# Performance work log

Measured on AMD Instinct MI355X. Metric: run time of the kernel, lower is better.

The kernel has to match this reference:

```python
import jax, jax.numpy as jnp
import numpy as np

HID = 512       # hidden_dim (embed/LSTM input)
HDE = 512       # hidden_dim_de == attn_channels (required by conv_att channel count)
NCLS = 7000
LSEQ = 40
B = 128
FH, FW = 8, 32


def setup_inputs() -> dict:
    key = jax.random.key(0)
    ks = jax.random.split(key, 16)
    s = 0.05
    inp = {
        "hidden_en": jax.random.normal(ks[0], (1, B, HID), jnp.float32),
        "x_em": jax.random.normal(ks[1], (B, HDE, FH, FW), jnp.float32),
        "att_x_em": jax.random.normal(ks[2], (B, FH * FW, HDE), jnp.float32),
        "target": jax.random.randint(ks[3], (B, LSEQ), 0, NCLS),
        "feature_h": FH,
        "feature_w": FW,
        # parameters
        "embed_w": jax.random.normal(ks[4], (NCLS, HID), jnp.float32) * s,
        "W_ih": jax.random.normal(ks[5], (4 * HDE, HID), jnp.float32) * s,   # LSTMCell input weights (i,f,g,o)
        "W_hh": jax.random.normal(ks[6], (4 * HDE, HDE), jnp.float32) * s,
        "b_ih": jax.random.normal(ks[7], (4 * HDE,), jnp.float32) * s,
        "b_hh": jax.random.normal(ks[8], (4 * HDE,), jnp.float32) * s,
        "hem_w": jax.random.normal(ks[9], (HDE, HDE), jnp.float32) * s,     # 1x1 conv h_em as matrix
        "hem_b": jax.random.normal(ks[10], (HDE,), jnp.float32) * s,
        "attw_w": jax.random.normal(ks[11], (HDE,), jnp.float32) * s,       # 1x1 conv conv_att -> 1 channel
        "attw_b": jax.random.normal(ks[12], (), jnp.float32) * s,
        "lin_w": jax.random.normal(ks[13], (NCLS, HDE + HDE), jnp.float32) * s,
        "lin_b": jax.random.normal(ks[14], (NCLS,), jnp.float32) * s,
    }
    return inp


def _decode(hidden_en, x_em, att_x_em, target, embed_w, W_ih, W_hh, b_ih, b_hh,
            hem_w, hem_b, attw_w, attw_b, lin_w, lin_b):
    L = target.shape[1]
    # teacher-forced inputs: step 0 uses hidden_en[-1], step t>=1 uses embed(target[:, t-1])
    xt0 = hidden_en[-1]                                   # [B, HID]
    xts = jnp.concatenate([xt0[None], jnp.transpose(embed_w[target[:, : L - 1]], (1, 0, 2))], axis=0)  # [L,B,HID]
    xg_all = jnp.einsum('lbi,gi->lbg', xts, W_ih) + b_ih  # precompute input gates [L,B,4H]
    Bn = x_em.shape[0]
    h0 = jnp.zeros((Bn, HDE), x_em.dtype)
    c0 = jnp.zeros((Bn, HDE), x_em.dtype)

    def step(carry, xg):
        h, c = carry
        gates = xg + h @ W_hh.T + b_hh
        i, f, g, o = jnp.split(gates, 4, axis=-1)
        c = jax.nn.sigmoid(f) * c + jax.nn.sigmoid(i) * jnp.tanh(g)
        h = jax.nn.sigmoid(o) * jnp.tanh(c)
        # additive attention (dropout treated as identity for determinism)
        hem = h @ hem_w.T + hem_b                          # [B, C]
        feat = jnp.tanh(x_em + hem[:, :, None, None])      # [B, C, H, W]
        feat_att = jnp.einsum('bchw,c->bhw', feat, attw_w) + attw_b
        alpha = jax.nn.softmax(feat_att.reshape(Bn, -1), axis=-1)  # [B, HW]
        att = jnp.einsum('bn,bnd->bd', alpha, att_x_em)    # [B, C]
        scores = jax.nn.log_softmax(jnp.concatenate([h, att], -1) @ lin_w.T + lin_b)
        return (h, c), scores

    _, ys = jax.lax.scan(step, (h0, c0), xg_all)           # ys: [L, B, NCLS]
    return jnp.transpose(ys, (1, 0, 2))                    # [B, L, NCLS]


def reference(hidden_en, x_em, att_x_em, target, feature_h, feature_w,
              embed_w, W_ih, W_hh, b_ih, b_hh, hem_w, hem_b, attw_w, attw_b,
              lin_w, lin_b):
    return _decode(hidden_en, x_em, att_x_em, target, embed_w, W_ih, W_hh,
                   b_ih, b_hh, hem_w, hem_b, attw_w, attw_b, lin_w, lin_b)
```

## Files before the change

kernel.cpp:

```cpp
#include <hip/hip_runtime.h>

#define B_    128
#define HIDD  512
#define NCLS  7000
#define NPAD  7040
#define LSEQ  40
#define MROWS 5120
#define TT    10

typedef __attribute__((ext_vector_type(8))) short bf16x8;
typedef __attribute__((ext_vector_type(4))) float f32x4;

__device__ __forceinline__ unsigned short f2bf(float x) {
  union { float f; unsigned u; } v; v.f = x;
  unsigned r = v.u + 0x7fffu + ((v.u >> 16) & 1u);
  return (unsigned short)(r >> 16);
}
__device__ __forceinline__ float bf2f(unsigned short h) {
  union { unsigned u; float f; } v; v.u = ((unsigned)h) << 16;
  return v.f;
}
__device__ __forceinline__ float sigm(float x) { return 1.f / (1.f + __expf(-x)); }
__device__ __forceinline__ float tanh_f(float x) {
  float e = __expf(2.f * x);
  return 1.f - 2.f / (e + 1.f);
}
__device__ __forceinline__ float rcp_f(float x) { return __builtin_amdgcn_rcpf(x); }

__global__ __launch_bounds__(256) void k_cvt(const float* __restrict__ src,
                                             unsigned short* __restrict__ dst, int n4) {
  int i = blockIdx.x * 256 + threadIdx.x;
  if (i >= n4) return;
  float4 v = ((const float4*)src)[i];
  ushort4 o; o.x = f2bf(v.x); o.y = f2bf(v.y); o.z = f2bf(v.z); o.w = f2bf(v.w);
  ((ushort4*)dst)[i] = o;
}

__global__ __launch_bounds__(256) void k_expcvt(const float* __restrict__ src,
                                                unsigned short* __restrict__ dst, int n4) {
  int i = blockIdx.x * 256 + threadIdx.x;
  if (i >= n4) return;
  float4 v = ((const float4*)src)[i];
  ushort4 o;
  o.x = f2bf(__expf(2.f * v.x)); o.y = f2bf(__expf(2.f * v.y));
  o.z = f2bf(__expf(2.f * v.z)); o.w = f2bf(__expf(2.f * v.w));
  ((ushort4*)dst)[i] = o;
}

__global__ __launch_bounds__(256) void k_linpad(const float* __restrict__ lw,
                                                unsigned short* __restrict__ dst) {
  int i = blockIdx.x * 256 + threadIdx.x;
  int e = i * 4;
  int row = e >> 10;
  ushort4 o;
  if (row < NCLS) {
    float4 v = *(const float4*)(lw + (size_t)row * 1024 + (e & 1023));
    o.x = f2bf(v.x); o.y = f2bf(v.y); o.z = f2bf(v.z); o.w = f2bf(v.w);
  } else { o.x = 0; o.y = 0; o.z = 0; o.w = 0; }
  ((ushort4*)dst)[i] = o;
}

__global__ __launch_bounds__(256) void k_xts(const float* __restrict__ hidden_en,
                                             const float* __restrict__ embed_w,
                                             const int* __restrict__ target,
                                             unsigned short* __restrict__ xts) {
  int i = blockIdx.x * 256 + threadIdx.x;
  int e = i * 4;
  int r = e >> 9, col = e & 511;
  int l = r >> 7, b = r & 127;
  const float* src;
  if (l == 0) src = hidden_en + b * 512 + col;
  else        src = embed_w + (size_t)target[b * LSEQ + (l - 1)] * 512 + col;
  float4 v = *(const float4*)src;
  ushort4 o; o.x = f2bf(v.x); o.y = f2bf(v.y); o.z = f2bf(v.z); o.w = f2bf(v.w);
  ((ushort4*)xts)[i] = o;
}

template <int MODE>
__global__ __launch_bounds__(256) void k_gemm(const unsigned short* __restrict__ A, int lda,
                                              const unsigned short* __restrict__ Bw, int ldb,
                                              const float* __restrict__ bias,
                                              void* __restrict__ outp, int ldc, int K) {
  __shared__ __align__(16) unsigned short As[128 * 32];
  __shared__ __align__(16) unsigned short Bs[128 * 32];
  const int tid = threadIdx.x;
  const int lane = tid & 63, wid = tid >> 6;
  const int wm = wid >> 1, wn = wid & 1;
  const int quad = lane >> 4, l16 = lane & 15;
  const int m0 = blockIdx.x * 128, n0 = blockIdx.y * 128;
  f32x4 acc[4][4];
#pragma unroll
  for (int i = 0; i < 4; i++)
#pragma unroll
    for (int j = 0; j < 4; j++) acc[i][j] = (f32x4){0.f, 0.f, 0.f, 0.f};

  const int r0 = tid >> 2, kq0 = (tid & 3) * 8;
  for (int k0 = 0; k0 < K; k0 += 32) {
#pragma unroll
    for (int s = 0; s < 2; s++) {
      int row = r0 + s * 64;
      *(bf16x8*)(As + row * 32 + kq0) = *(const bf16x8*)(A + (size_t)(m0 + row) * lda + k0 + kq0);
      *(bf16x8*)(Bs + row * 32 + kq0) = *(const bf16x8*)(Bw + (size_t)(n0 + row) * ldb + k0 + kq0);
    }
    __syncthreads();
    bf16x8 af[4], bfr[4];
#pragma unroll
    for (int i = 0; i < 4; i++)
      af[i] = *(const bf16x8*)(As + (wm * 64 + i * 16 + l16) * 32 + quad * 8);
#pragma unroll
    for (int j = 0; j < 4; j++)
      bfr[j] = *(const bf16x8*)(Bs + (wn * 64 + j * 16 + l16) * 32 + quad * 8);
#pragma unroll
    for (int i = 0; i < 4; i++)
#pragma unroll
      for (int j = 0; j < 4; j++)
        acc[i][j] = __builtin_amdgcn_mfma_f32_16x16x32_bf16(af[i], bfr[j], acc[i][j], 0, 0, 0);
    __syncthreads();
  }
#pragma unroll
  for (int i = 0; i < 4; i++) {
    int mbase = m0 + wm * 64 + i * 16 + quad * 4;
#pragma unroll
    for (int j = 0; j < 4; j++) {
      int n = n0 + wn * 64 + j * 16 + l16;
#pragma unroll
      for (int r = 0; r < 4; r++) {
        float v = acc[i][j][r];
        int m = mbase + r;
        if (MODE == 0) {
          ((unsigned short*)outp)[(size_t)m * ldc + n] = f2bf(v + bias[n]);
        } else if (MODE == 3) {
          ((float*)outp)[(size_t)m * ldc + n] = __expf(2.f * (v + bias[n]));
        } else {
          if (n < NCLS) {
            int t = m >> 7, b = m & 127;
            ((float*)outp)[((size_t)(b * LSEQ + t)) * NCLS + n] = v + bias[n];
          }
        }
      }
    }
  }
}

__global__ __launch_bounds__(256) void k_gates(const float* __restrict__ h_prev,
                                               float* __restrict__ h_new,
                                               float* __restrict__ c_buf,
                                               const unsigned short* __restrict__ xg,
                                               const float* __restrict__ W_hh,
                                               const float* __restrict__ b_hh,
                                               unsigned short* __restrict__ hatt, int t) {
  __shared__ float h_s[16][68];
  __shared__ float W_s[64][68];
  const int tid = threadIdx.x;
  const int mt = blockIdx.x >> 5, jt = blockIdx.x & 31;
  const int m0 = mt * 16, j0 = jt * 16;
  const int mi = tid >> 4, ji = tid & 15;
  float a0 = 0.f, a1 = 0.f, a2 = 0.f, a3 = 0.f;
  if (t > 0) {
    for (int k0 = 0; k0 < 512; k0 += 64) {
      {
        int row = tid >> 4, c4 = (tid & 15) * 4;
        *(float4*)&h_s[row][c4] = *(const float4*)&h_prev[(m0 + row) * 512 + k0 + c4];
      }
#pragma unroll
      for (int w = 0; w < 4; w++) {
        int lin = w * 256 + tid;
        int row = lin >> 4, c4 = (lin & 15) * 4;
        int g = row >> 4, jj = row & 15;
        *(float4*)&W_s[row][c4] = *(const float4*)&W_hh[(size_t)((g << 9) + j0 + jj) * 512 + k0 + c4];
      }
      __syncthreads();
#pragma unroll 4
      for (int kk = 0; kk < 64; kk += 4) {
        float4 hv = *(const float4*)&h_s[mi][kk];
        float4 w0 = *(const float4*)&W_s[ji][kk];
        float4 w1 = *(const float4*)&W_s[16 + ji][kk];
        float4 w2 = *(const float4*)&W_s[32 + ji][kk];
        float4 w3 = *(const float4*)&W_s[48 + ji][kk];
        a0 += hv.x * w0.x + hv.y * w0.y + hv.z * w0.z + hv.w * w0.w;
        a1 += hv.x * w1.x + hv.y * w1.y + hv.z * w1.z + hv.w * w1.w;
        a2 += hv.x * w2.x + hv.y * w2.y + hv.z * w2.z + hv.w * w2.w;
        a3 += hv.x * w3.x + hv.y * w3.y + hv.z * w3.z + hv.w * w3.w;
      }
      __syncthreads();
    }
  }
  const int m = m0 + mi, j = j0 + ji;
  const size_t r = (size_t)t * 128 + m;
  a0 += bf2f(xg[r * 2048 + j])          + b_hh[j];
  a1 += bf2f(xg[r * 2048 + 512 + j])    + b_hh[512 + j];
  a2 += bf2f(xg[r * 2048 + 1024 + j])   + b_hh[1024 + j];
  a3 += bf2f(xg[r * 2048 + 1536 + j])   + b_hh[1536 + j];
  float ig = sigm(a0), fg = sigm(a1), gg = tanh_f(a2), og = sigm(a3);
  float c_old = (t > 0) ? c_buf[m * 512 + j] : 0.f;
  float c = fg * c_old + ig * gg;
  float h = og * tanh_f(c);
  c_buf[m * 512 + j] = c;
  h_new[m * 512 + j] = h;
  hatt[r * 1024 + j] = f2bf(h);
}

__global__ __launch_bounds__(256) void k_feat(const float* __restrict__ Eh,
                                              const unsigned short* __restrict__ Ex,
                                              const float* __restrict__ attw_w,
                                              float* __restrict__ s_all) {
  __shared__ float EhL[TT][512];
  __shared__ float wL[512];
  const int tid = threadIdx.x;
  const int tg = blockIdx.x >> 7, b = blockIdx.x & 127;
  const int t0 = tg * TT;
  for (int i = tid * 4; i < TT * 512; i += 1024) {
    int t = i >> 9, c = i & 511;
    *(float4*)&EhL[t][c] = *(const float4*)&Eh[((size_t)(t0 + t) * 128 + b) * 512 + c];
  }
  if (tid < 128) *(float4*)&wL[tid * 4] = *(const float4*)&attw_w[tid * 4];
  __syncthreads();
  const int p = tid;
  const unsigned short* xp = Ex + (size_t)b * 512 * 256 + p;
  float acc[TT];
#pragma unroll
  for (int t = 0; t < TT; t++) acc[t] = 0.f;
  for (int c0 = 0; c0 < 512; c0 += 4) {
    float ex0 = bf2f(xp[(size_t)(c0 + 0) * 256]);
    float ex1 = bf2f(xp[(size_t)(c0 + 1) * 256]);
    float ex2 = bf2f(xp[(size_t)(c0 + 2) * 256]);
    float ex3 = bf2f(xp[(size_t)(c0 + 3) * 256]);
    float4 wv = *(const float4*)&wL[c0];
#pragma unroll
    for (int t = 0; t < TT; t++) {
      float4 eh = *(const float4*)&EhL[t][c0];
      acc[t] = __builtin_fmaf(wv.x, rcp_f(__builtin_fmaf(ex0, eh.x, 1.f)), acc[t]);
      acc[t] = __builtin_fmaf(wv.y, rcp_f(__builtin_fmaf(ex1, eh.y, 1.f)), acc[t]);
      acc[t] = __builtin_fmaf(wv.z, rcp_f(__builtin_fmaf(ex2, eh.z, 1.f)), acc[t]);
      acc[t] = __builtin_fmaf(wv.w, rcp_f(__builtin_fmaf(ex3, eh.w, 1.f)), acc[t]);
    }
  }
#pragma unroll
  for (int t = 0; t < TT; t++)
    s_all[((size_t)(t0 + t) * 128 + b) * 256 + p] = -2.f * acc[t];
}

__global__ __launch_bounds__(256) void k_att(const float* __restrict__ s_all,
                                             const float* __restrict__ atx,
                                             unsigned short* __restrict__ hatt) {
  __shared__ float sL[40][257];
  __shared__ float zinv[40];
  const int tid = threadIdx.x;
  const int b = blockIdx.x >> 1, dh = blockIdx.x & 1;
  for (int i = tid; i < 40 * 256; i += 256) {
    int t = i >> 8, p = i & 255;
    sL[t][p] = s_all[((size_t)t * 128 + b) * 256 + p];
  }
  __syncthreads();
  if (tid < 40) {
    int t = tid;
    float mx = -1e30f;
    for (int p = 0; p < 256; p++) mx = fmaxf(mx, sL[t][p]);
    float z = 0.f;
    for (int p = 0; p < 256; p++) { float e = __expf(sL[t][p] - mx); sL[t][p] = e; z += e; }
    zinv[t] = 1.f / z;
  }
  __syncthreads();
  float acc[40];
#pragma unroll
  for (int t = 0; t < 40; t++) acc[t] = 0.f;
  const int d = dh * 256 + tid;
  const float* ap = atx + (size_t)b * 256 * 512 + d;
  for (int p = 0; p < 256; p++) {
    float av = ap[(size_t)p * 512];
#pragma unroll
    for (int t = 0; t < 40; t++) acc[t] += sL[t][p] * av;
  }
#pragma unroll
  for (int t = 0; t < 40; t++) {
    float v = acc[t] * zinv[t];
    hatt[((size_t)t * 128 + b) * 1024 + 512 + d] = f2bf(v);
  }
}

__global__ __launch_bounds__(256) void k_lsm(float* __restrict__ out) {
  __shared__ float buf[7000];
  __shared__ float red[256];
  const int tid = threadIdx.x;
  float* pr = out + (size_t)blockIdx.x * NCLS;
  for (int i = tid * 4; i < NCLS; i += 1024)
    *(float4*)&buf[i] = *(const float4*)&pr[i];
  __syncthreads();
  float mx = -1e30f;
  for (int i = tid; i < NCLS; i += 256) mx = fmaxf(mx, buf[i]);
  red[tid] = mx; __syncthreads();
  for (int s = 128; s > 0; s >>= 1) { if (tid < s) red[tid] = fmaxf(red[tid], red[tid + s]); __syncthreads(); }
  mx = red[0]; __syncthreads();
  float sum = 0.f;
  for (int i = tid; i < NCLS; i += 256) sum += __expf(buf[i] - mx);
  red[tid] = sum; __syncthreads();
  for (int s = 128; s > 0; s >>= 1) { if (tid < s) red[tid] += red[tid + s]; __syncthreads(); }
  float lse = mx + __logf(red[0]);
  for (int i = tid * 4; i < NCLS; i += 1024) {
    float4 v = *(const float4*)&buf[i];
    v.x -= lse; v.y -= lse; v.z -= lse; v.w -= lse;
    *(float4*)&pr[i] = v;
  }
}

extern "C" void kernel_launch(void* const* d_in, const int* in_sizes, int n_in,
                              void* d_out, int out_size, void* d_ws, size_t ws_size,
                              hipStream_t stream) {
  const float* hidden_en = (const float*)d_in[0];
  const float* x_em      = (const float*)d_in[1];
  const float* att_x     = (const float*)d_in[2];
  const int*   target    = (const int*)d_in[3];
  const float* embed_w   = (const float*)d_in[6];
  const float* W_ih      = (const float*)d_in[7];
  const float* W_hh      = (const float*)d_in[8];
  const float* b_ih      = (const float*)d_in[9];
  const float* b_hh      = (const float*)d_in[10];
  const float* hem_w     = (const float*)d_in[11];
  const float* hem_b     = (const float*)d_in[12];
  const float* attw_w    = (const float*)d_in[13];
  const float* lin_w     = (const float*)d_in[15];
  const float* lin_b     = (const float*)d_in[16];
  float* out = (float*)d_out;
  (void)in_sizes; (void)n_in; (void)out_size; (void)ws_size;

  char* w = (char*)d_ws;
  size_t off = 0;
  auto alloc = [&](size_t bytes) { char* p = w + off; off = (off + bytes + 255) & ~(size_t)255; return p; };
  unsigned short* xts  = (unsigned short*)alloc((size_t)MROWS * 512 * 2);
  unsigned short* wih  = (unsigned short*)alloc((size_t)2048 * 512 * 2);
  unsigned short* xg   = (unsigned short*)alloc((size_t)MROWS * 2048 * 2);
  unsigned short* hemw = (unsigned short*)alloc((size_t)512 * 512 * 2);
  unsigned short* linw = (unsigned short*)alloc((size_t)NPAD * 1024 * 2);
  unsigned short* xem  = (unsigned short*)alloc((size_t)128 * 512 * 256 * 2);
  unsigned short* hatt = (unsigned short*)alloc((size_t)MROWS * 1024 * 2);
  float* h0      = (float*)alloc((size_t)128 * 512 * 4);
  float* h1      = (float*)alloc((size_t)128 * 512 * 4);
  float* cb      = (float*)alloc((size_t)128 * 512 * 4);
  float* eh_all  = (float*)alloc((size_t)MROWS * 512 * 4);
  float* s_all   = (float*)alloc((size_t)MROWS * 256 * 4);

  k_cvt<<<1024, 256, 0, stream>>>(W_ih, wih, 2048 * 512 / 4);
  k_cvt<<<256, 256, 0, stream>>>(hem_w, hemw, 512 * 512 / 4);
  k_expcvt<<<16384, 256, 0, stream>>>(x_em, xem, 128 * 512 * 256 / 4);
  k_linpad<<<NPAD * 1024 / 4 / 256, 256, 0, stream>>>(lin_w, linw);
  k_xts<<<MROWS * 512 / 4 / 256, 256, 0, stream>>>(hidden_en, embed_w, target, xts);
  k_gemm<0><<<dim3(40, 16), 256, 0, stream>>>(xts, 512, wih, 512, b_ih, xg, 2048, 512);

  for (int t = 0; t < LSEQ; t++) {
    const float* hp = (t & 1) ? h0 : h1;
    float* hn = (t & 1) ? h1 : h0;
    k_gates<<<256, 256, 0, stream>>>(hp, hn, cb, xg, W_hh, b_hh, hatt, t);
  }

  k_gemm<3><<<dim3(40, 4), 256, 0, stream>>>(hatt, 1024, hemw, 512, hem_b, eh_all, 512, 512);
  k_feat<<<512, 256, 0, stream>>>(eh_all, xem, attw_w, s_all);
  k_att<<<256, 256, 0, stream>>>(s_all, att_x, hatt);

  k_gemm<2><<<dim3(40, 55), 256, 0, stream>>>(hatt, 1024, linw, 1024, lin_b, out, NCLS, 1024);
  k_lsm<<<MROWS, 256, 0, stream>>>(out);
}
```

Baseline: 1.395 ms.

## Fuse LSTM recurrence into one persistent kernel with grid barrier and bf16 MFMA

Replaces the 40 per-step k_gates launches with a single persistent kernel of 32 workgroups that loops over time steps. Steps are synchronised through a global atomic barrier. The recurrent matmul now uses bf16 MFMA on a pre-swizzled W_hh, and the hidden state is kept in bf16 while the cell state stays in LDS. This removes per-step launch overhead and the fp32 scalar FMA work. The cost is lower recurrent precision and a spin barrier that depends on all 32 blocks being resident at once.

```diff
diff --git a/kernel.cpp b/kernel.cpp
--- a/kernel.cpp
+++ b/kernel.cpp
@@ -76,6 +76,112 @@
   ((ushort4*)xts)[i] = o;
 }
 
+__global__ __launch_bounds__(256) void k_wprep(const float* __restrict__ W_hh,
+                                               unsigned short* __restrict__ Wb) {
+  int idx = blockIdx.x * 256 + threadIdx.x;
+  int lane = idx & 63, kg = (idx >> 6) & 15, g = (idx >> 10) & 3, jwb = idx >> 12;
+  int l16 = lane & 15, quad = lane >> 4;
+  const float* src = W_hh + (size_t)(g * 512 + jwb * 16 + l16) * 512 + kg * 32 + quad * 8;
+  float4 v0 = *(const float4*)src, v1 = *(const float4*)(src + 4);
+  unsigned short o[8] = {f2bf(v0.x), f2bf(v0.y), f2bf(v0.z), f2bf(v0.w),
+                         f2bf(v1.x), f2bf(v1.y), f2bf(v1.z), f2bf(v1.w)};
+  *(ushort4*)(Wb + (size_t)idx * 8)     = *(ushort4*)o;
+  *(ushort4*)(Wb + (size_t)idx * 8 + 4) = *(ushort4*)(o + 4);
+}
+
+__global__ void k_binit(unsigned* bar) { bar[0] = 0; bar[1] = 0; }
+
+__global__ __launch_bounds__(1024) void k_scan(const unsigned short* __restrict__ xg,
+                                               const unsigned short* __restrict__ Wb,
+                                               const float* __restrict__ b_hh,
+                                               unsigned short* __restrict__ hG,
+                                               unsigned short* __restrict__ hatt,
+                                               unsigned* __restrict__ bar) {
+  __shared__ __align__(16) char uS[34816];
+  unsigned short* hs = (unsigned short*)uS;
+  float* gsum = (float*)uS;
+  __shared__ float cS[2048];
+  __shared__ float bhL[64];
+  const int tid = threadIdx.x;
+  const int lane = tid & 63, wid = tid >> 6;
+  const int l16 = lane & 15, quad = lane >> 4;
+  const int mt2 = wid & 3, g = wid >> 2;
+  const int jwb = blockIdx.x, jw = jwb * 16;
+  if (tid < 64) bhL[tid] = b_hh[(tid >> 4) * 512 + jw + (tid & 15)];
+  __syncthreads();
+  for (int t = 0; t < LSEQ; t++) {
+    if (t > 0) {
+      f32x4 acc0 = {0.f, 0.f, 0.f, 0.f}, acc1 = {0.f, 0.f, 0.f, 0.f};
+      for (int k0 = 0; k0 < 512; k0 += 128) {
+#pragma unroll
+        for (int pass = 0; pass < 2; pass++) {
+          int i = pass * 1024 + tid;
+          int row = i >> 4, kc = (i & 15) << 3;
+          *(bf16x8*)&hs[row * 136 + kc] = *(const bf16x8*)&hG[row * 512 + k0 + kc];
+        }
+        __syncthreads();
+#pragma unroll
+        for (int kk = 0; kk < 4; kk++) {
+          int kg = (k0 >> 5) + kk;
+          bf16x8 b  = *(const bf16x8*)&Wb[((((size_t)jwb * 4 + g) * 16 + kg) * 64 + lane) * 8];
+          bf16x8 a0 = *(const bf16x8*)&hs[(mt2 * 32 + l16) * 136 + kk * 32 + quad * 8];
+          bf16x8 a1 = *(const bf16x8*)&hs[(mt2 * 32 + 16 + l16) * 136 + kk * 32 + quad * 8];
+          acc0 = __builtin_amdgcn_mfma_f32_16x16x32_bf16(a0, b, acc0, 0, 0, 0);
+          acc1 = __builtin_amdgcn_mfma_f32_16x16x32_bf16(a1, b, acc1, 0, 0, 0);
+        }
+        __syncthreads();
+      }
+#pragma unroll
+      for (int r = 0; r < 4; r++) {
+        gsum[g * 2176 + (mt2 * 32 + quad * 4 + r) * 17 + l16]      = acc0[r];
+        gsum[g * 2176 + (mt2 * 32 + 16 + quad * 4 + r) * 17 + l16] = acc1[r];
+      }
+      __syncthreads();
+    }
+#pragma unroll
+    for (int half = 0; half < 2; half++) {
+      int e = half * 1024 + tid;
+      int m = e >> 4, jj = e & 15;
+      size_t xr = ((size_t)t * 128 + m) * 2048 + jw + jj;
+      float a0 = bf2f(xg[xr])        + bhL[jj];
+      float a1 = bf2f(xg[xr + 512])  + bhL[16 + jj];
+      float a2 = bf2f(xg[xr + 1024]) + bhL[32 + jj];
+      float a3 = bf2f(xg[xr + 1536]) + bhL[48 + jj];
+      float c_old = 0.f;
+      if (t > 0) {
+        a0 += gsum[m * 17 + jj];
+        a1 += gsum[2176 + m * 17 + jj];
+        a2 += gsum[2 * 2176 + m * 17 + jj];
+        a3 += gsum[3 * 2176 + m * 17 + jj];
+        c_old = cS[e];
+      }
+      float c = sigm(a1) * c_old + sigm(a0) * tanh_f(a2);
+      float h = sigm(a3) * tanh_f(c);
+      cS[e] = c;
+      unsigned short hb = f2bf(h);
+      hG[m * 512 + jw + jj] = hb;
+      hatt[((size_t)t * 128 + m) * 1024 + jw + jj] = hb;
+    }
+    if (t < LSEQ - 1) {
+      __threadfence();
+      __syncthreads();
+      if (tid == 0) {
+        unsigned gen = __hip_atomic_load(&bar[1], __ATOMIC_RELAXED, __HIP_MEMORY_SCOPE_AGENT);
+        unsigned a = __hip_atomic_fetch_add(&bar[0], 1u, __ATOMIC_ACQ_REL, __HIP_MEMORY_SCOPE_AGENT);
+        if (a == 31u) {
+          __hip_atomic_store(&bar[0], 0u, __ATOMIC_RELAXED, __HIP_MEMORY_SCOPE_AGENT);
+          __hip_atomic_store(&bar[1], gen + 1u, __ATOMIC_RELEASE, __HIP_MEMORY_SCOPE_AGENT);
+        } else {
+          while (__hip_atomic_load(&bar[1], __ATOMIC_ACQUIRE, __HIP_MEMORY_SCOPE_AGENT) == gen)
+            __builtin_amdgcn_s_sleep(2);
+        }
+      }
+      __syncthreads();
+      __threadfence();
+    }
+  }
+}
+
 template <int MODE>
 __global__ __launch_bounds__(256) void k_gemm(const unsigned short* __restrict__ A, int lda,
                                               const unsigned short* __restrict__ Bw, int ldb,
@@ -140,64 +246,6 @@
       }
     }
   }
-}
-
-__global__ __launch_bounds__(256) void k_gates(const float* __restrict__ h_prev,
-                                               float* __restrict__ h_new,
-                                               float* __restrict__ c_buf,
-                                               const unsigned short* __restrict__ xg,
-                                               const float* __restrict__ W_hh,
-                                               const float* __restrict__ b_hh,
-                                               unsigned short* __restrict__ hatt, int t) {
-  __shared__ float h_s[16][68];
-  __shared__ float W_s[64][68];
-  const int tid = threadIdx.x;
-  const int mt = blockIdx.x >> 5, jt = blockIdx.x & 31;
-  const int m0 = mt * 16, j0 = jt * 16;
-  const int mi = tid >> 4, ji = tid & 15;
-  float a0 = 0.f, a1 = 0.f, a2 = 0.f, a3 = 0.f;
-  if (t > 0) {
-    for (int k0 = 0; k0 < 512; k0 += 64) {
-      {
-        int row = tid >> 4, c4 = (tid & 15) * 4;
-        *(float4*)&h_s[row][c4] = *(const float4*)&h_prev[(m0 + row) * 512 + k0 + c4];
-      }
-#pragma unroll
-      for (int w = 0; w < 4; w++) {
-        int lin = w * 256 + tid;
-        int row = lin >> 4, c4 = (lin & 15) * 4;
-        int g = row >> 4, jj = row & 15;
-        *(float4*)&W_s[row][c4] = *(const float4*)&W_hh[(size_t)((g << 9) + j0 + jj) * 512 + k0 + c4];
-      }
-      __syncthreads();
-#pragma unroll 4
-      for (int kk = 0; kk < 64; kk += 4) {
-        float4 hv = *(const float4*)&h_s[mi][kk];
-        float4 w0 = *(const float4*)&W_s[ji][kk];
-        float4 w1 = *(const float4*)&W_s[16 + ji][kk];
-        float4 w2 = *(const float4*)&W_s[32 + ji][kk];
-        float4 w3 = *(const float4*)&W_s[48 + ji][kk];
-        a0 += hv.x * w0.x + hv.y * w0.y + hv.z * w0.z + hv.w * w0.w;
-        a1 += hv.x * w1.x + hv.y * w1.y + hv.z * w1.z + hv.w * w1.w;
-        a2 += hv.x * w2.x + hv.y * w2.y + hv.z * w2.z + hv.w * w2.w;
-        a3 += hv.x * w3.x + hv.y * w3.y + hv.z * w3.z + hv.w * w3.w;
-      }
-      __syncthreads();
-    }
-  }
-  const int m = m0 + mi, j = j0 + ji;
-  const size_t r = (size_t)t * 128 + m;
-  a0 += bf2f(xg[r * 2048 + j])          + b_hh[j];
-  a1 += bf2f(xg[r * 2048 + 512 + j])    + b_hh[512 + j];
-  a2 += bf2f(xg[r * 2048 + 1024 + j])   + b_hh[1024 + j];
-  a3 += bf2f(xg[r * 2048 + 1536 + j])   + b_hh[1536 + j];
-  float ig = sigm(a0), fg = sigm(a1), gg = tanh_f(a2), og = sigm(a3);
-  float c_old = (t > 0) ? c_buf[m * 512 + j] : 0.f;
-  float c = fg * c_old + ig * gg;
-  float h = og * tanh_f(c);
-  c_buf[m * 512 + j] = c;
-  h_new[m * 512 + j] = h;
-  hatt[r * 1024 + j] = f2bf(h);
 }
 
 __global__ __launch_bounds__(256) void k_feat(const float* __restrict__ Eh,
@@ -333,9 +381,9 @@
   unsigned short* linw = (unsigned short*)alloc((size_t)NPAD * 1024 * 2);
   unsigned short* xem  = (unsigned short*)alloc((size_t)128 * 512 * 256 * 2);
   unsigned short* hatt = (unsigned short*)alloc((size_t)MROWS * 1024 * 2);
-  float* h0      = (float*)alloc((size_t)128 * 512 * 4);
-  float* h1      = (float*)alloc((size_t)128 * 512 * 4);
-  float* cb      = (float*)alloc((size_t)128 * 512 * 4);
+  unsigned short* wb   = (unsigned short*)alloc((size_t)2048 * 512 * 2);
+  unsigned short* hG   = (unsigned short*)alloc((size_t)128 * 512 * 2);
+  unsigned*       bar  = (unsigned*)alloc(256);
   float* eh_all  = (float*)alloc((size_t)MROWS * 512 * 4);
   float* s_all   = (float*)alloc((size_t)MROWS * 256 * 4);
 
@@ -344,13 +392,11 @@
   k_expcvt<<<16384, 256, 0, stream>>>(x_em, xem, 128 * 512 * 256 / 4);
   k_linpad<<<NPAD * 1024 / 4 / 256, 256, 0, stream>>>(lin_w, linw);
   k_xts<<<MROWS * 512 / 4 / 256, 256, 0, stream>>>(hidden_en, embed_w, target, xts);
+  k_wprep<<<512, 256, 0, stream>>>(W_hh, wb);
+  k_binit<<<1, 1, 0, stream>>>(bar);
   k_gemm<0><<<dim3(40, 16), 256, 0, stream>>>(xts, 512, wih, 512, b_ih, xg, 2048, 512);
 
-  for (int t = 0; t < LSEQ; t++) {
-    const float* hp = (t & 1) ? h0 : h1;
-    float* hn = (t & 1) ? h1 : h0;
-    k_gates<<<256, 256, 0, stream>>>(hp, hn, cb, xg, W_hh, b_hh, hatt, t);
-  }
+  k_scan<<<32, 1024, 0, stream>>>(xg, wb, b_hh, hG, hatt, bar);
 
   k_gemm<3><<<dim3(40, 4), 256, 0, stream>>>(hatt, 1024, hemw, 512, hem_b, eh_all, 512, 512);
   k_feat<<<512, 256, 0, stream>>>(eh_all, xem, attw_w, s_all);
```

After: 1.885 ms. 1.35x slower.

## Replace FP32 LSTM recurrence kernel with bf16 MFMA step kernel

Applied to the files above, without the earlier changes.

Swaps the per-step fp32 scalar-FMA gate kernel (256 blocks) for an MFMA bf16 kernel that computes a 128x128 tile of all four gates per block (16 blocks), using a W_hh copy pre-converted to bf16 and reordered so each block's gate rows are contiguous. h is kept in bf16 and the cell state moves to a block-private layout zeroed up front, so the t==0 branch is gone. Gate outputs are staged through shared memory for the elementwise LSTM update. This cuts FLOP cost per step but uses only 16 blocks with no k-loop pipelining, and bf16 recurrent state lowers precision.

```diff
diff --git a/kernel.cpp b/kernel.cpp
--- a/kernel.cpp
+++ b/kernel.cpp
@@ -34,6 +34,11 @@
   float4 v = ((const float4*)src)[i];
   ushort4 o; o.x = f2bf(v.x); o.y = f2bf(v.y); o.z = f2bf(v.z); o.w = f2bf(v.w);
   ((ushort4*)dst)[i] = o;
+}
+
+__global__ __launch_bounds__(256) void k_zero(float4* __restrict__ dst, int n4) {
+  int i = blockIdx.x * 256 + threadIdx.x;
+  if (i < n4) dst[i] = (float4){0.f, 0.f, 0.f, 0.f};
 }
 
 __global__ __launch_bounds__(256) void k_expcvt(const float* __restrict__ src,
@@ -74,6 +79,99 @@
   float4 v = *(const float4*)src;
   ushort4 o; o.x = f2bf(v.x); o.y = f2bf(v.y); o.z = f2bf(v.z); o.w = f2bf(v.w);
   ((ushort4*)xts)[i] = o;
+}
+
+__global__ __launch_bounds__(256) void k_wprep(const float* __restrict__ W_hh,
+                                               unsigned short* __restrict__ Wp) {
+  int i = blockIdx.x * 256 + threadIdx.x;
+  int e = i * 4;
+  int rp = e >> 9, k = e & 511;
+  int jb = rp >> 7, rr = rp & 127, g = rr >> 5, jj = rr & 31;
+  const float* src = W_hh + (size_t)(g * 512 + jb * 32 + jj) * 512 + k;
+  float4 v = *(const float4*)src;
+  ushort4 o; o.x = f2bf(v.x); o.y = f2bf(v.y); o.z = f2bf(v.z); o.w = f2bf(v.w);
+  ((ushort4*)Wp)[i] = o;
+}
+
+__global__ __launch_bounds__(256) void k_step(const unsigned short* __restrict__ hin,
+                                              unsigned short* __restrict__ hout,
+                                              const unsigned short* __restrict__ Wp,
+                                              const unsigned short* __restrict__ xg,
+                                              const float* __restrict__ b_hh,
+                                              float* __restrict__ cG,
+                                              unsigned short* __restrict__ hatt, int t) {
+  __shared__ __align__(16) char uS[34816];
+  unsigned short* As = (unsigned short*)uS;
+  unsigned short* Bs = (unsigned short*)(uS + 8192);
+  float* gbuf = (float*)uS;
+  __shared__ float biasL[128];
+  const int tid = threadIdx.x;
+  const int lane = tid & 63, wid = tid >> 6;
+  const int wm = wid >> 1, wn = wid & 1;
+  const int quad = lane >> 4, l16 = lane & 15;
+  const int jb = blockIdx.x, jw = jb * 32;
+  if (tid < 128) biasL[tid] = b_hh[(tid >> 5) * 512 + jw + (tid & 31)];
+
+  f32x4 acc[4][4];
+#pragma unroll
+  for (int i = 0; i < 4; i++)
+#pragma unroll
+    for (int j = 0; j < 4; j++) acc[i][j] = (f32x4){0.f, 0.f, 0.f, 0.f};
+
+  const unsigned short* Bw = Wp + (size_t)jb * 128 * 512;
+  const int r0 = tid >> 2, kq0 = (tid & 3) * 8;
+  for (int k0 = 0; k0 < 512; k0 += 32) {
+#pragma unroll
+    for (int s = 0; s < 2; s++) {
+      int row = r0 + s * 64;
+      *(bf16x8*)(As + row * 32 + kq0) = *(const bf16x8*)(hin + (size_t)row * 512 + k0 + kq0);
+      *(bf16x8*)(Bs + row * 32 + kq0) = *(const bf16x8*)(Bw + (size_t)row * 512 + k0 + kq0);
+    }
+    __syncthreads();
+    bf16x8 af[4], bfr[4];
+#pragma unroll
+    for (int i = 0; i < 4; i++)
+      af[i] = *(const bf16x8*)(As + (wm * 64 + i * 16 + l16) * 32 + quad * 8);
+#pragma unroll
+    for (int j = 0; j < 4; j++)
+      bfr[j] = *(const bf16x8*)(Bs + (wn * 64 + j * 16 + l16) * 32 + quad * 8);
+#pragma unroll
+    for (int i = 0; i < 4; i++)
+#pragma unroll
+      for (int j = 0; j < 4; j++)
+        acc[i][j] = __builtin_amdgcn_mfma_f32_16x16x32_bf16(af[i], bfr[j], acc[i][j], 0, 0, 0);
+    __syncthreads();
+  }
+#pragma unroll
+  for (int half = 0; half < 2; half++) {
+    if (wm == half) {
+#pragma unroll
+      for (int i = 0; i < 4; i++)
+#pragma unroll
+        for (int j = 0; j < 4; j++)
+#pragma unroll
+          for (int r = 0; r < 4; r++)
+            gbuf[(i * 16 + quad * 4 + r) * 136 + wn * 64 + j * 16 + l16] = acc[i][j][r];
+    }
+    __syncthreads();
+    for (int e = tid; e < 2048; e += 256) {
+      int ml = e >> 5, jj = e & 31;
+      int m = half * 64 + ml;
+      size_t xr = ((size_t)t * 128 + m) * 2048 + jw + jj;
+      float a0 = gbuf[ml * 136 + jj]      + bf2f(xg[xr])        + biasL[jj];
+      float a1 = gbuf[ml * 136 + 32 + jj] + bf2f(xg[xr + 512])  + biasL[32 + jj];
+      float a2 = gbuf[ml * 136 + 64 + jj] + bf2f(xg[xr + 1024]) + biasL[64 + jj];
+      float a3 = gbuf[ml * 136 + 96 + jj] + bf2f(xg[xr + 1536]) + biasL[96 + jj];
+      size_t ci = (size_t)(jb * 128 + m) * 32 + jj;
+      float c = sigm(a1) * cG[ci] + sigm(a0) * tanh_f(a2);
+      float h = sigm(a3) * tanh_f(c);
+      cG[ci] = c;
+      unsigned short hb = f2bf(h);
+      hout[(size_t)m * 512 + jw + jj] = hb;
+      hatt[((size_t)t * 128 + m) * 1024 + jw + jj] = hb;
+    }
+    __syncthreads();
+  }
 }
 
 template <int MODE>
@@ -140,64 +238,6 @@
       }
     }
   }
-}
-
-__global__ __launch_bounds__(256) void k_gates(const float* __restrict__ h_prev,
-                                               float* __restrict__ h_new,
-                                               float* __restrict__ c_buf,
-                                               const unsigned short* __restrict__ xg,
-                                               const float* __restrict__ W_hh,
-                                               const float* __restrict__ b_hh,
-                                               unsigned short* __restrict__ hatt, int t) {
-  __shared__ float h_s[16][68];
-  __shared__ float W_s[64][68];
-  const int tid = threadIdx.x;
-  const int mt = blockIdx.x >> 5, jt = blockIdx.x & 31;
-  const int m0 = mt * 16, j0 = jt * 16;
-  const int mi = tid >> 4, ji = tid & 15;
-  float a0 = 0.f, a1 = 0.f, a2 = 0.f, a3 = 0.f;
-  if (t > 0) {
-    for (int k0 = 0; k0 < 512; k0 += 64) {
-      {
-        int row = tid >> 4, c4 = (tid & 15) * 4;
-        *(float4*)&h_s[row][c4] = *(const float4*)&h_prev[(m0 + row) * 512 + k0 + c4];
-      }
-#pragma unroll
-      for (int w = 0; w < 4; w++) {
-        int lin = w * 256 + tid;
-        int row = lin >> 4, c4 = (lin & 15) * 4;
-        int g = row >> 4, jj = row & 15;
-        *(float4*)&W_s[row][c4] = *(const float4*)&W_hh[(size_t)((g << 9) + j0 + jj) * 512 + k0 + c4];
-      }
-      __syncthreads();
-#pragma unroll 4
-      for (int kk = 0; kk < 64; kk += 4) {
-        float4 hv = *(const float4*)&h_s[mi][kk];
-        float4 w0 = *(const float4*)&W_s[ji][kk];
-        float4 w1 = *(const float4*)&W_s[16 + ji][kk];
-        float4 w2 = *(const float4*)&W_s[32 + ji][kk];
-        float4 w3 = *(const float4*)&W_s[48 + ji][kk];
-        a0 += hv.x * w0.x + hv.y * w0.y + hv.z * w0.z + hv.w * w0.w;
-        a1 += hv.x * w1.x + hv.y * w1.y + hv.z * w1.z + hv.w * w1.w;
-        a2 += hv.x * w2.x + hv.y * w2.y + hv.z * w2.z + hv.w * w2.w;
-        a3 += hv.x * w3.x + hv.y * w3.y + hv.z * w3.z + hv.w * w3.w;
-      }
-      __syncthreads();
-    }
-  }
-  const int m = m0 + mi, j = j0 + ji;
-  const size_t r = (size_t)t * 128 + m;
-  a0 += bf2f(xg[r * 2048 + j])          + b_hh[j];
-  a1 += bf2f(xg[r * 2048 + 512 + j])    + b_hh[512 + j];
-  a2 += bf2f(xg[r * 2048 + 1024 + j])   + b_hh[1024 + j];
-  a3 += bf2f(xg[r * 2048 + 1536 + j])   + b_hh[1536 + j];
-  float ig = sigm(a0), fg = sigm(a1), gg = tanh_f(a2), og = sigm(a3);
-  float c_old = (t > 0) ? c_buf[m * 512 + j] : 0.f;
-  float c = fg * c_old + ig * gg;
-  float h = og * tanh_f(c);
-  c_buf[m * 512 + j] = c;
-  h_new[m * 512 + j] = h;
-  hatt[r * 1024 + j] = f2bf(h);
 }
 
 __global__ __launch_bounds__(256) void k_feat(const float* __restrict__ Eh,
@@ -333,9 +373,11 @@
   unsigned short* linw = (unsigned short*)alloc((size_t)NPAD * 1024 * 2);
   unsigned short* xem  = (unsigned short*)alloc((size_t)128 * 512 * 256 * 2);
   unsigned short* hatt = (unsigned short*)alloc((size_t)MROWS * 1024 * 2);
-  float* h0      = (float*)alloc((size_t)128 * 512 * 4);
-  float* h1      = (float*)alloc((size_t)128 * 512 * 4);
-  float* cb      = (float*)alloc((size_t)128 * 512 * 4);
+  unsigned short* wp   = (unsigned short*)alloc((size_t)2048 * 512 * 2);
+  char* zreg = alloc(131072 + 262144);
+  unsigned short* hG0 = (unsigned short*)zreg;
+  float*          cG  = (float*)(zreg + 131072);
+  unsigned short* hG1 = (unsigned short*)alloc((size_t)128 * 512 * 2);
   float* eh_all  = (float*)alloc((size_t)MROWS * 512 * 4);
   float* s_all   = (float*)alloc((size_t)MROWS * 256 * 4);
 
@@ -344,12 +386,14 @@
   k_expcvt<<<16384, 256, 0, stream>>>(x_em, xem, 128 * 512 * 256 / 4);
   k_linpad<<<NPAD * 1024 / 4 / 256, 256, 0, stream>>>(lin_w, linw);
   k_xts<<<MROWS * 512 / 4 / 256, 256, 0, stream>>>(hidden_en, embed_w, target, xts);
+  k_wprep<<<1024, 256, 0, stream>>>(W_hh, wp);
+  k_zero<<<96, 256, 0, stream>>>((float4*)zreg, (131072 + 262144) / 16);
   k_gemm<0><<<dim3(40, 16), 256, 0, stream>>>(xts, 512, wih, 512, b_ih, xg, 2048, 512);
 
   for (int t = 0; t < LSEQ; t++) {
-    const float* hp = (t & 1) ? h0 : h1;
-    float* hn = (t & 1) ? h1 : h0;
-    k_gates<<<256, 256, 0, stream>>>(hp, hn, cb, xg, W_hh, b_hh, hatt, t);
+    const unsigned short* hin = (t & 1) ? hG1 : hG0;
+    unsigned short* hout      = (t & 1) ? hG0 : hG1;
+    k_step<<<16, 256, 0, stream>>>(hin, hout, wp, xg, b_hh, cG, hatt, t);
   }
 
   k_gemm<3><<<dim3(40, 4), 256, 0, stream>>>(hatt, 1024, hemw, 512, hem_b, eh_all, 512, 512);
```

Result: slower. 1.457 ms (+4.5%).
